# Kernel tuning notes

Measured on AMD Instinct MI355X. Metric: run time of the kernel, lower is better.

The kernel has to match this reference:

```python
import jax, jax.numpy as jnp
import numpy as np

OUT = 7            # output_size
SR = 2             # sampling_ratio (samples per bin per axis)
SCALES = (0.25, 0.125, 0.0625, 0.03125)
CANON_SIZE = 224.0
CANON_LVL = 4.0
MIN_LVL = 2
IMG = 800.0


def setup_inputs() -> dict:
    key = jax.random.key(0)
    kf = jax.random.split(key, 6)
    B, C, R = 2, 256, 256
    sizes = [200, 100, 50, 25]
    feats = [jax.random.normal(kf[i], (B, C, s, s), jnp.float32) for i, s in enumerate(sizes)]
    # valid xyxy boxes in [0, IMG], log-uniform side lengths -> spread across FPN levels
    ctr = jax.random.uniform(kf[4], (B, R, 2), minval=0.0, maxval=IMG)
    wh = jnp.exp(jax.random.uniform(kf[5], (B, R, 2), minval=float(np.log(16.0)), maxval=float(np.log(512.0))))
    lo = jnp.clip(ctr - wh / 2, 0.0, IMG)
    hi = jnp.clip(ctr + wh / 2, 0.0, IMG)
    boxes = jnp.concatenate([lo, hi], axis=-1)  # [B,R,4]
    return {"feat0": feats[0], "feat1": feats[1], "feat2": feats[2], "feat3": feats[3], "boxes": boxes}


def _prep(c, lim):
    """torchvision ROIAlign (aligned=False) bilinear index prep.
    c: sample coords [N,OUT,SR]; lim: per-box feature extent (H or W) [N]."""
    limb = lim[:, None, None]
    valid = (c > -1.0) & (c < limb)          # out-of-range samples contribute 0
    cc = jnp.maximum(c, 0.0)
    low = jnp.floor(cc)
    cap = limb - 1.0
    at_edge = low >= cap                      # y_low >= H-1 -> clamp, frac = 0
    low = jnp.minimum(low, cap)
    high = jnp.minimum(low + 1.0, cap)
    cc = jnp.where(at_edge, low, cc)
    frac = cc - low
    return valid, low.astype(jnp.int32), high.astype(jnp.int32), frac


def roi_pooler(feats, boxes):
    B, R = boxes.shape[0], boxes.shape[1]
    C = feats[0].shape[1]
    N = B * R
    flat = boxes.reshape(N, 4)
    bidx = jnp.repeat(jnp.arange(B, dtype=jnp.int32), R)  # batch index per ROI

    # level assignment (assign_boxes_to_levels)
    area = (flat[:, 2] - flat[:, 0]) * (flat[:, 3] - flat[:, 1])
    lvl = jnp.floor(CANON_LVL + jnp.log2(jnp.sqrt(area) / CANON_SIZE + 1e-8))
    lvl = jnp.clip(lvl, MIN_LVL, MIN_LVL + len(feats) - 1).astype(jnp.int32) - MIN_LVL  # [N] in [0,3]

    # pad all levels to P2 size and stack so each ROI is sampled once at its level
    Hm, Wm = feats[0].shape[2], feats[0].shape[3]
    padded = jnp.stack([jnp.pad(f, ((0, 0), (0, 0), (0, Hm - f.shape[2]), (0, Wm - f.shape[3]))) for f in feats])
    fp = padded.transpose(0, 1, 3, 4, 2)  # [L,B,Hm,Wm,C] channels-last for gather
    Hs = jnp.array([f.shape[2] for f in feats], jnp.float32)[lvl]
    Ws = jnp.array([f.shape[3] for f in feats], jnp.float32)[lvl]
    scale = jnp.array(SCALES, jnp.float32)[lvl]

    # ROIAlign aligned=False: scale coords, clamp roi size to >= 1
    x1 = flat[:, 0] * scale
    y1 = flat[:, 1] * scale
    x2 = flat[:, 2] * scale
    y2 = flat[:, 3] * scale
    roi_w = jnp.maximum(x2 - x1, 1.0)
    roi_h = jnp.maximum(y2 - y1, 1.0)
    bw = roi_w / OUT
    bh = roi_h / OUT

    # sample grid: bin index + sub-sample offsets -> [N,OUT,SR]
    grid = jnp.arange(OUT, dtype=jnp.float32)[None, :, None] + (jnp.arange(SR, dtype=jnp.float32)[None, None, :] + 0.5) / SR
    ys = y1[:, None, None] + bh[:, None, None] * grid
    xs = x1[:, None, None] + bw[:, None, None] * grid

    vy, yl, yh, fy = _prep(ys, Hs)
    vx, xl, xh, fx = _prep(xs, Ws)

    P = OUT * OUT * SR * SR  # all sample points per ROI

    def by(a):  # y-axis quantity -> broadcast over (out_y,out_x,sr_y,sr_x)
        return jnp.broadcast_to(a[:, :, None, :, None], (N, OUT, OUT, SR, SR)).reshape(N, P)

    def bx(a):
        return jnp.broadcast_to(a[:, None, :, None, :], (N, OUT, OUT, SR, SR)).reshape(N, P)

    YL, YH, FY, VY = by(yl), by(yh), by(fy), by(vy)
    XL, XH, FX, VX = bx(xl), bx(xh), bx(fx), bx(vx)

    li = lvl[:, None]
    bi = bidx[:, None]
    v00 = fp[li, bi, YL, XL]  # [N,P,C]
    v01 = fp[li, bi, YL, XH]
    v10 = fp[li, bi, YH, XL]
    v11 = fp[li, bi, YH, XH]

    w = lambda a: a[..., None]
    val = (w((1 - FY) * (1 - FX)) * v00 + w((1 - FY) * FX) * v01
           + w(FY * (1 - FX)) * v10 + w(FY * FX) * v11)
    val = val * w((VY & VX).astype(val.dtype))
    out = val.reshape(N, OUT, OUT, SR * SR, C).mean(axis=3)  # average over SR*SR samples
    return out.transpose(0, 3, 1, 2)  # [N,C,OUT,OUT]


def reference(feat0, feat1, feat2, feat3, boxes):
    return roi_pooler([feat0, feat1, feat2, feat3], boxes)
```

## Files before the change

### kernel.cpp

```cpp
#include <hip/hip_runtime.h>
#include <math.h>

typedef unsigned short u16;
typedef unsigned int   u32;
typedef float f32x4 __attribute__((ext_vector_type(4)));

#define OUTSZ 7
#define B_ 2
#define C_ 256
#define R_ 256
#define N_ (B_ * R_)

#define PX_TOTAL 106250
#define WS_NEEDED ((size_t)PX_TOTAL * 256 * 2)

__device__ __forceinline__ u16 f2bf(float v) {
    u32 u = __float_as_uint(v);
    u += 0x7fffu + ((u >> 16) & 1u);
    return (u16)(u >> 16);
}

__device__ __forceinline__ u32 pack2bf(float a, float b) {
    return (u32)f2bf(a) | ((u32)f2bf(b) << 16);
}

__global__ __launch_bounds__(256, 8) void nhwc_cast(
    const float* __restrict__ f0, const float* __restrict__ f1,
    const float* __restrict__ f2, const float* __restrict__ f3,
    u16* __restrict__ dst)
{
    __shared__ u32 lds32[128 * 32];
    const int tid  = threadIdx.x;
    const int lane = tid & 63;
    const int wave = tid >> 6;

    const int t  = blockIdx.x;
    const int cb = blockIdx.y;
    const int b  = blockIdx.z;
    const float* src; int HWsz, dstBase, ft;
    if      (t < 157) { src = f0; HWsz = 40000; dstBase = 0;      ft = t;       }
    else if (t < 197) { src = f1; HWsz = 10000; dstBase = 80000;  ft = t - 157; }
    else if (t < 207) { src = f2; HWsz = 2500;  dstBase = 100000; ft = t - 197; }
    else              { src = f3; HWsz = 625;   dstBase = 105000; ft = t - 207; }

    const int fbase = ft * 256;
    const int cw    = cb * 64 + wave * 16;
    const int rem   = HWsz - fbase;
    const int p0    = 4 * lane;
    const bool vec  = ((HWsz & 3) == 0) && (p0 + 3 < rem);

    const float* base = src + ((size_t)(b * C_ + cw)) * HWsz + fbase;

    float f[16][4];
    #pragma unroll
    for (int i = 0; i < 16; ++i) {
        const float* row = base + (size_t)i * HWsz;
        if (vec) {
            f32x4 v = __builtin_nontemporal_load((const f32x4*)(row + p0));
            f[i][0] = v.x; f[i][1] = v.y; f[i][2] = v.z; f[i][3] = v.w;
        } else {
            #pragma unroll
            for (int k = 0; k < 4; ++k)
                f[i][k] = (p0 + k < rem) ? row[p0 + k] : 0.0f;
        }
    }

    const int half  = lane >> 5;
    const int pl0   = p0 & 127;
    const int maxpx = rem < 256 ? rem : 256;

    #pragma unroll
    for (int h = 0; h < 2; ++h) {
        if (half == h) {
            #pragma unroll
            for (int r = 0; r < 2; ++r) {
                #pragma unroll
                for (int j = 0; j < 4; ++j) {
                    uint4 o;
                    o.x = pack2bf(f[r * 8 + 0][j], f[r * 8 + 1][j]);
                    o.y = pack2bf(f[r * 8 + 2][j], f[r * 8 + 3][j]);
                    o.z = pack2bf(f[r * 8 + 4][j], f[r * 8 + 5][j]);
                    o.w = pack2bf(f[r * 8 + 6][j], f[r * 8 + 7][j]);
                    const int q = (wave * 2 + r) ^ (lane & 7);
                    *(uint4*)&lds32[(pl0 + j) * 32 + q * 4] = o;
                }
            }
        }
        __syncthreads();

        #pragma unroll
        for (int i = 0; i < 4; ++i) {
            const int idx = i * 256 + tid;
            const int pxl = idx >> 3;
            const int sub = idx & 7;
            const int px  = h * 128 + pxl;
            if (px < maxpx) {
                const int q = sub ^ ((pxl >> 2) & 7);
                uint4 o = *(const uint4*)&lds32[pxl * 32 + q * 4];
                *(uint4*)(dst + (size_t)(dstBase + b * HWsz + fbase + px) * 256 + cb * 64 + sub * 8) = o;
            }
        }
        if (h == 0) __syncthreads();
    }
}

__device__ __forceinline__ void acc4(float4& a, uint2 u, float w) {
    a.x += w * __uint_as_float(u.x << 16);
    a.y += w * __uint_as_float(u.x & 0xffff0000u);
    a.z += w * __uint_as_float(u.y << 16);
    a.w += w * __uint_as_float(u.y & 0xffff0000u);
}

template<int NC, int CB>
__device__ __forceinline__ void store_out(const float* lds, float* out, int n) {
    #pragma unroll 4
    for (int i = threadIdx.x; i < 256 * NC; i += 256) {
        const int c = i / NC;
        const int j = i - c * NC;
        __builtin_nontemporal_store(lds[j * 260 + c],
                                    out + ((size_t)(n * C_ + c)) * 49 + CB + j);
    }
}

__global__ __launch_bounds__(256) void roi_gather(
    const u16* __restrict__ ws16, const float* __restrict__ boxes,
    float* __restrict__ out)
{
    __shared__ float lds[28 * 260];
    __shared__ float s_wy0[14], s_wy1[14], s_wx0[14], s_wx1[14];
    __shared__ int   s_yl[14], s_yh[14], s_xl[14], s_xh[14];
    __shared__ int   s_base, s_W;

    const int g    = blockIdx.x;
    const int n    = blockIdx.y;
    const int tid  = threadIdx.x;
    const int lane = tid & 63;
    const int wave = tid >> 6;

    if (tid < 28) {
        const float* bx = boxes + (size_t)n * 4;
        float x1 = bx[0], y1 = bx[1], x2 = bx[2], y2 = bx[3];
        float area = (x2 - x1) * (y2 - y1);
        float lf = floorf(4.0f + log2f(sqrtf(area) / 224.0f + 1e-8f));
        lf = fminf(fmaxf(lf, 2.0f), 5.0f);
        int lvl = (int)lf - 2;
        const float scales[4] = {0.25f, 0.125f, 0.0625f, 0.03125f};
        const int   sizes[4]  = {200, 100, 50, 25};
        const int   bases[4]  = {0, 80000, 100000, 105000};
        float scale = scales[lvl];
        int   HW    = sizes[lvl];
        float lim = (float)HW, cap = lim - 1.0f;
        float fx1 = x1 * scale, fy1 = y1 * scale;
        float bw = fmaxf(x2 * scale - fx1, 1.0f) / (float)OUTSZ;
        float bh = fmaxf(y2 * scale - fy1, 1.0f) / (float)OUTSZ;
        if (tid == 0) { s_base = bases[lvl] + (n >> 8) * HW * HW; s_W = HW; }

        const int  i   = (tid < 14) ? tid : tid - 14;
        const bool isy = tid < 14;
        float o  = isy ? fy1 : fx1;
        float st = isy ? bh  : bw;
        float gq = (float)(i >> 1) + ((float)(i & 1) + 0.5f) * 0.5f;
        float c = o + st * gq;
        bool  v = (c > -1.0f) && (c < lim);
        float cc = fmaxf(c, 0.0f);
        float low = floorf(cc);
        bool  edge = low >= cap;
        low = fminf(low, cap);
        float high = fminf(low + 1.0f, cap);
        float fr = edge ? 0.0f : (cc - low);
        float w0 = v ? (1.0f - fr) : 0.0f;
        float w1 = v ? fr : 0.0f;
        if (isy) { s_yl[i] = (int)low; s_yh[i] = (int)high; s_wy0[i] = w0; s_wy1[i] = w1; }
        else     { s_xl[i] = (int)low; s_xh[i] = (int)high; s_wx0[i] = w0; s_wx1[i] = w1; }
    }
    __syncthreads();

    const int base = s_base, W = s_W;
    const int CB = g ? 28 : 0;
    const int NC = g ? 21 : 28;

    for (int cell = CB + wave; cell < CB + NC; cell += 4) {
        const int cu = __builtin_amdgcn_readfirstlane(cell);
        const int oy = cu / 7, ox = cu - oy * 7;
        float4 acc = {0.0f, 0.0f, 0.0f, 0.0f};
        #pragma unroll
        for (int sy = 0; sy < 2; ++sy) {
            const int ei = oy * 2 + sy;
            const float wy0 = s_wy0[ei], wy1 = s_wy1[ei];
            const int rl = base + s_yl[ei] * W;
            const int rh = base + s_yh[ei] * W;
            #pragma unroll
            for (int sx = 0; sx < 2; ++sx) {
                const int ej = ox * 2 + sx;
                const float w00 = wy0 * s_wx0[ej], w01 = wy0 * s_wx1[ej];
                const float w10 = wy1 * s_wx0[ej], w11 = wy1 * s_wx1[ej];
                const int xl = s_xl[ej], xh = s_xh[ej];
                uint2 u00 = ((const uint2*)(ws16 + (size_t)(rl + xl) * 256))[lane];
                uint2 u01 = ((const uint2*)(ws16 + (size_t)(rl + xh) * 256))[lane];
                uint2 u10 = ((const uint2*)(ws16 + (size_t)(rh + xl) * 256))[lane];
                uint2 u11 = ((const uint2*)(ws16 + (size_t)(rh + xh) * 256))[lane];
                acc4(acc, u00, w00);
                acc4(acc, u01, w01);
                acc4(acc, u10, w10);
                acc4(acc, u11, w11);
            }
        }
        acc.x *= 0.25f; acc.y *= 0.25f; acc.z *= 0.25f; acc.w *= 0.25f;
        *(float4*)&lds[(cell - CB) * 260 + 4 * lane] = acc;
    }
    __syncthreads();

    if (g == 0) store_out<28, 0>(lds, out, n);
    else        store_out<21, 28>(lds, out, n);
}

__global__ __launch_bounds__(256) void roi_direct(
    const float* __restrict__ f0, const float* __restrict__ f1,
    const float* __restrict__ f2, const float* __restrict__ f3,
    const float* __restrict__ boxes, float* __restrict__ out)
{
    const int total = B_ * R_ * C_ * OUTSZ * OUTSZ;
    int idx = blockIdx.x * blockDim.x + threadIdx.x;
    if (idx >= total) return;
    int ox = idx % 7, oy = (idx / 7) % 7, c = (idx / 49) % C_, n = idx / (49 * C_), b = n >> 8;
    const float* bx = boxes + (size_t)n * 4;
    float x1 = bx[0], y1 = bx[1], x2 = bx[2], y2 = bx[3];
    float lf = floorf(4.0f + log2f(sqrtf((x2 - x1) * (y2 - y1)) / 224.0f + 1e-8f));
    int lvl = (int)fminf(fmaxf(lf, 2.0f), 5.0f) - 2;
    const float scales[4] = {0.25f, 0.125f, 0.0625f, 0.03125f};
    const int sizes[4] = {200, 100, 50, 25};
    float scale = scales[lvl]; int HW = sizes[lvl];
    const float* fl = lvl == 0 ? f0 : lvl == 1 ? f1 : lvl == 2 ? f2 : f3;
    float fx1 = x1 * scale, fy1 = y1 * scale;
    float bw = fmaxf(x2 * scale - fx1, 1.0f) / 7.0f, bh = fmaxf(y2 * scale - fy1, 1.0f) / 7.0f;
    const float* plane = fl + ((size_t)(b * C_ + c)) * HW * HW;
    float lim = (float)HW, cap = lim - 1.0f, acc = 0.0f;
    #pragma unroll
    for (int sy = 0; sy < 2; sy++) {
        float yc = fy1 + bh * ((float)oy + ((float)sy + 0.5f) * 0.5f);
        bool vy = (yc > -1.0f) && (yc < lim);
        float ccy = fmaxf(yc, 0.0f), lowy = floorf(ccy);
        bool ey = lowy >= cap; lowy = fminf(lowy, cap);
        float highy = fminf(lowy + 1.0f, cap);
        float wfy = ey ? 0.0f : (ccy - lowy);
        int yl = (int)lowy, yh = (int)highy;
        #pragma unroll
        for (int sx = 0; sx < 2; sx++) {
            float xc = fx1 + bw * ((float)ox + ((float)sx + 0.5f) * 0.5f);
            bool vx = (xc > -1.0f) && (xc < lim);
            float ccx = fmaxf(xc, 0.0f), lowx = floorf(ccx);
            bool ex = lowx >= cap; lowx = fminf(lowx, cap);
            float highx = fminf(lowx + 1.0f, cap);
            float wfx = ex ? 0.0f : (ccx - lowx);
            int xl = (int)lowx, xh = (int)highx;
            if (vy && vx) {
                float v00 = plane[yl * HW + xl], v01 = plane[yl * HW + xh];
                float v10 = plane[yh * HW + xl], v11 = plane[yh * HW + xh];
                acc += (1.0f - wfy) * ((1.0f - wfx) * v00 + wfx * v01)
                     + wfy * ((1.0f - wfx) * v10 + wfx * v11);
            }
        }
    }
    out[idx] = acc * 0.25f;
}

extern "C" void kernel_launch(void* const* d_in, const int* in_sizes, int n_in,
                              void* d_out, int out_size, void* d_ws, size_t ws_size,
                              hipStream_t stream) {
    const float* f0    = (const float*)d_in[0];
    const float* f1    = (const float*)d_in[1];
    const float* f2    = (const float*)d_in[2];
    const float* f3    = (const float*)d_in[3];
    const float* boxes = (const float*)d_in[4];
    float* out = (float*)d_out;

    if (ws_size < WS_NEEDED) {
        const int total = B_ * R_ * C_ * OUTSZ * OUTSZ;
        roi_direct<<<(total + 255) / 256, 256, 0, stream>>>(f0, f1, f2, f3, boxes, out);
        return;
    }

    u16* nhwc = (u16*)d_ws;

    nhwc_cast<<<dim3(210, 4, 2), 256, 0, stream>>>(f0, f1, f2, f3, nhwc);
    roi_gather<<<dim3(2, N_), 256, 0, stream>>>(nhwc, boxes, out);
}
```

Baseline: 205.8 us.

## Split ROI gather by channel halves and widen NHWC cast blocks

The gather kernel now splits work by channel halves (128 channels per block) instead of by output cells. Each block handles all 49 cells and writes its contiguous output slab with float4 stores, replacing the strided scalar nontemporal stores. The cast kernel moves to 512-thread blocks with 8 channels per wave, doing a single LDS transpose pass with one barrier, and drops nontemporal loads. The trade-off is narrower 4-byte gathers per lane instead of 8-byte ones, LDS writes strided by 49 that may bank-conflict, and a larger LDS footprint in the cast kernel.

```diff
diff --git a/kernel.cpp b/kernel.cpp
--- a/kernel.cpp
+++ b/kernel.cpp
@@ -3,7 +3,6 @@
 
 typedef unsigned short u16;
 typedef unsigned int   u32;
-typedef float f32x4 __attribute__((ext_vector_type(4)));
 
 #define OUTSZ 7
 #define B_ 2
@@ -24,12 +23,12 @@
     return (u32)f2bf(a) | ((u32)f2bf(b) << 16);
 }
 
-__global__ __launch_bounds__(256, 8) void nhwc_cast(
+__global__ __launch_bounds__(512, 8) void nhwc_cast(
     const float* __restrict__ f0, const float* __restrict__ f1,
     const float* __restrict__ f2, const float* __restrict__ f3,
     u16* __restrict__ dst)
 {
-    __shared__ u32 lds32[128 * 32];
+    __shared__ u32 lds32[256 * 32];
     const int tid  = threadIdx.x;
     const int lane = tid & 63;
     const int wave = tid >> 6;
@@ -44,19 +43,19 @@
     else              { src = f3; HWsz = 625;   dstBase = 105000; ft = t - 207; }
 
     const int fbase = ft * 256;
-    const int cw    = cb * 64 + wave * 16;
+    const int cw    = cb * 64 + wave * 8;
     const int rem   = HWsz - fbase;
     const int p0    = 4 * lane;
     const bool vec  = ((HWsz & 3) == 0) && (p0 + 3 < rem);
 
     const float* base = src + ((size_t)(b * C_ + cw)) * HWsz + fbase;
 
-    float f[16][4];
-    #pragma unroll
-    for (int i = 0; i < 16; ++i) {
+    float f[8][4];
+    #pragma unroll
+    for (int i = 0; i < 8; ++i) {
         const float* row = base + (size_t)i * HWsz;
         if (vec) {
-            f32x4 v = __builtin_nontemporal_load((const f32x4*)(row + p0));
+            float4 v = *(const float4*)(row + p0);
             f[i][0] = v.x; f[i][1] = v.y; f[i][2] = v.z; f[i][3] = v.w;
         } else {
             #pragma unroll
@@ -65,60 +64,29 @@
         }
     }
 
-    const int half  = lane >> 5;
-    const int pl0   = p0 & 127;
+    #pragma unroll
+    for (int j = 0; j < 4; ++j) {
+        uint4 o;
+        o.x = pack2bf(f[0][j], f[1][j]);
+        o.y = pack2bf(f[2][j], f[3][j]);
+        o.z = pack2bf(f[4][j], f[5][j]);
+        o.w = pack2bf(f[6][j], f[7][j]);
+        const int q = wave ^ (lane & 7);
+        *(uint4*)&lds32[(p0 + j) * 32 + q * 4] = o;
+    }
+    __syncthreads();
+
     const int maxpx = rem < 256 ? rem : 256;
-
-    #pragma unroll
-    for (int h = 0; h < 2; ++h) {
-        if (half == h) {
-            #pragma unroll
-            for (int r = 0; r < 2; ++r) {
-                #pragma unroll
-                for (int j = 0; j < 4; ++j) {
-                    uint4 o;
-                    o.x = pack2bf(f[r * 8 + 0][j], f[r * 8 + 1][j]);
-                    o.y = pack2bf(f[r * 8 + 2][j], f[r * 8 + 3][j]);
-                    o.z = pack2bf(f[r * 8 + 4][j], f[r * 8 + 5][j]);
-                    o.w = pack2bf(f[r * 8 + 6][j], f[r * 8 + 7][j]);
-                    const int q = (wave * 2 + r) ^ (lane & 7);
-                    *(uint4*)&lds32[(pl0 + j) * 32 + q * 4] = o;
-                }
-            }
-        }
-        __syncthreads();
-
-        #pragma unroll
-        for (int i = 0; i < 4; ++i) {
-            const int idx = i * 256 + tid;
-            const int pxl = idx >> 3;
-            const int sub = idx & 7;
-            const int px  = h * 128 + pxl;
-            if (px < maxpx) {
-                const int q = sub ^ ((pxl >> 2) & 7);
-                uint4 o = *(const uint4*)&lds32[pxl * 32 + q * 4];
-                *(uint4*)(dst + (size_t)(dstBase + b * HWsz + fbase + px) * 256 + cb * 64 + sub * 8) = o;
-            }
-        }
-        if (h == 0) __syncthreads();
-    }
-}
-
-__device__ __forceinline__ void acc4(float4& a, uint2 u, float w) {
-    a.x += w * __uint_as_float(u.x << 16);
-    a.y += w * __uint_as_float(u.x & 0xffff0000u);
-    a.z += w * __uint_as_float(u.y << 16);
-    a.w += w * __uint_as_float(u.y & 0xffff0000u);
-}
-
-template<int NC, int CB>
-__device__ __forceinline__ void store_out(const float* lds, float* out, int n) {
-    #pragma unroll 4
-    for (int i = threadIdx.x; i < 256 * NC; i += 256) {
-        const int c = i / NC;
-        const int j = i - c * NC;
-        __builtin_nontemporal_store(lds[j * 260 + c],
-                                    out + ((size_t)(n * C_ + c)) * 49 + CB + j);
+    #pragma unroll
+    for (int i = 0; i < 4; ++i) {
+        const int idx = i * 512 + tid;
+        const int px  = idx >> 3;
+        const int sub = idx & 7;
+        if (px < maxpx) {
+            const int q = sub ^ ((px >> 2) & 7);
+            uint4 o = *(const uint4*)&lds32[px * 32 + q * 4];
+            *(uint4*)(dst + (size_t)(dstBase + b * HWsz + fbase + px) * 256 + cb * 64 + sub * 8) = o;
+        }
     }
 }
 
@@ -126,7 +94,7 @@
     const u16* __restrict__ ws16, const float* __restrict__ boxes,
     float* __restrict__ out)
 {
-    __shared__ float lds[28 * 260];
+    __shared__ float lds[128 * 49];
     __shared__ float s_wy0[14], s_wy1[14], s_wx0[14], s_wx1[14];
     __shared__ int   s_yl[14], s_yh[14], s_xl[14], s_xh[14];
     __shared__ int   s_base, s_W;
@@ -176,13 +144,12 @@
     __syncthreads();
 
     const int base = s_base, W = s_W;
-    const int CB = g ? 28 : 0;
-    const int NC = g ? 21 : 28;
-
-    for (int cell = CB + wave; cell < CB + NC; cell += 4) {
+    const int c0 = g * 128;
+
+    for (int cell = wave; cell < 49; cell += 4) {
         const int cu = __builtin_amdgcn_readfirstlane(cell);
         const int oy = cu / 7, ox = cu - oy * 7;
-        float4 acc = {0.0f, 0.0f, 0.0f, 0.0f};
+        float a0 = 0.0f, a1 = 0.0f;
         #pragma unroll
         for (int sy = 0; sy < 2; ++sy) {
             const int ei = oy * 2 + sy;
@@ -195,23 +162,24 @@
                 const float w00 = wy0 * s_wx0[ej], w01 = wy0 * s_wx1[ej];
                 const float w10 = wy1 * s_wx0[ej], w11 = wy1 * s_wx1[ej];
                 const int xl = s_xl[ej], xh = s_xh[ej];
-                uint2 u00 = ((const uint2*)(ws16 + (size_t)(rl + xl) * 256))[lane];
-                uint2 u01 = ((const uint2*)(ws16 + (size_t)(rl + xh) * 256))[lane];
-                uint2 u10 = ((const uint2*)(ws16 + (size_t)(rh + xl) * 256))[lane];
-                uint2 u11 = ((const uint2*)(ws16 + (size_t)(rh + xh) * 256))[lane];
-                acc4(acc, u00, w00);
-                acc4(acc, u01, w01);
-                acc4(acc, u10, w10);
-                acc4(acc, u11, w11);
+                u32 u00 = ((const u32*)(ws16 + (size_t)(rl + xl) * 256 + c0))[lane];
+                u32 u01 = ((const u32*)(ws16 + (size_t)(rl + xh) * 256 + c0))[lane];
+                u32 u10 = ((const u32*)(ws16 + (size_t)(rh + xl) * 256 + c0))[lane];
+                u32 u11 = ((const u32*)(ws16 + (size_t)(rh + xh) * 256 + c0))[lane];
+                a0 += w00 * __uint_as_float(u00 << 16) + w01 * __uint_as_float(u01 << 16)
+                    + w10 * __uint_as_float(u10 << 16) + w11 * __uint_as_float(u11 << 16);
+                a1 += w00 * __uint_as_float(u00 & 0xffff0000u) + w01 * __uint_as_float(u01 & 0xffff0000u)
+                    + w10 * __uint_as_float(u10 & 0xffff0000u) + w11 * __uint_as_float(u11 & 0xffff0000u);
             }
         }
-        acc.x *= 0.25f; acc.y *= 0.25f; acc.z *= 0.25f; acc.w *= 0.25f;
-        *(float4*)&lds[(cell - CB) * 260 + 4 * lane] = acc;
+        lds[(2 * lane) * 49 + cu]     = a0 * 0.25f;
+        lds[(2 * lane + 1) * 49 + cu] = a1 * 0.25f;
     }
     __syncthreads();
 
-    if (g == 0) store_out<28, 0>(lds, out, n);
-    else        store_out<21, 28>(lds, out, n);
+    const float4* lv = (const float4*)lds;
+    float4* ov = (float4*)(out + ((size_t)(n * C_ + c0)) * 49);
+    for (int i = tid; i < 1568; i += 256) ov[i] = lv[i];
 }
 
 __global__ __launch_bounds__(256) void roi_direct(
@@ -282,6 +250,6 @@
 
     u16* nhwc = (u16*)d_ws;
 
-    nhwc_cast<<<dim3(210, 4, 2), 256, 0, stream>>>(f0, f1, f2, f3, nhwc);
+    nhwc_cast<<<dim3(210, 4, 2), 512, 0, stream>>>(f0, f1, f2, f3, nhwc);
     roi_gather<<<dim3(2, N_), 256, 0, stream>>>(nhwc, boxes, out);
 }
```

After: 180.8 us. 12.2% less time.
